# Kernel tuning notes

Hardware: AMD Instinct MI355X
Metric: run time of the kernel (lower is better)

## Reference

```python
import jax, jax.numpy as jnp
import numpy as np

ROI_SIZE = 7
MAX_BIN_H = 8   # max adaptive-maxpool bin height for crop H <= 37
MAX_BIN_W = 9   # max adaptive-maxpool bin width  for crop W <= 50
SCALE = 0.0625  # 1/16 feature stride


def setup_inputs() -> dict:
    key = jax.random.key(0)
    ks = jax.random.split(key, 12)
    B, C, h, w = 1, 512, 37, 50          # conv5 feature map of a 600x800 image
    N = 512                               # number of ROIs (proposals)
    n_class = 21
    d_in, d_fc = C * ROI_SIZE * ROI_SIZE, 4096
    x = jax.random.normal(ks[0], (B, C, h, w), dtype=jnp.float32)
    # rois in image coordinates (x1, y1, x2, y2), image is 800x600
    x1 = jax.random.uniform(ks[1], (N,), minval=0.0, maxval=700.0)
    y1 = jax.random.uniform(ks[2], (N,), minval=0.0, maxval=500.0)
    bw = jax.random.uniform(ks[3], (N,), minval=16.0, maxval=400.0)
    bh = jax.random.uniform(ks[4], (N,), minval=16.0, maxval=300.0)
    rois = jnp.stack([x1, y1, jnp.minimum(x1 + bw, 799.0), jnp.minimum(y1 + bh, 599.0)], axis=1).astype(jnp.float32)
    roi_index = jnp.zeros((N,), dtype=jnp.int32)  # single image in batch
    W1 = jax.random.normal(ks[5], (d_in, d_fc), dtype=jnp.float32) * 0.01
    b1 = jnp.zeros((d_fc,), dtype=jnp.float32)
    W2 = jax.random.normal(ks[6], (d_fc, d_fc), dtype=jnp.float32) * 0.01
    b2 = jnp.zeros((d_fc,), dtype=jnp.float32)
    Wp = jax.random.normal(ks[7], (d_fc, n_class * 4), dtype=jnp.float32) * 0.001
    bp = jax.random.normal(ks[8], (n_class * 4,), dtype=jnp.float32) * 0.001
    Ws = jax.random.normal(ks[9], (d_fc, n_class), dtype=jnp.float32) * 0.01
    bs = jax.random.normal(ks[10], (n_class,), dtype=jnp.float32) * 0.01
    return dict(x=x, rois=rois, roi_index=roi_index, W1=W1, b1=b1, W2=W2, b2=b2, Wp=Wp, bp=bp, Ws=Ws, bs=bs)


def _roi_pool(x, rois, roi_index):
    """Faithful port of roi_pooling(): per-ROI crop + AdaptiveMaxPool2d(7)."""
    B, C, h, w = x.shape
    S = ROI_SIZE
    coords = jnp.round(rois * SCALE)  # round-half-even, like torch.round
    cx1 = jnp.clip(coords[:, 0], 0, w).astype(jnp.int32)
    cy1 = jnp.clip(coords[:, 1], 0, h).astype(jnp.int32)
    cx2 = jnp.clip(coords[:, 2], 0, w).astype(jnp.int32)
    cy2 = jnp.clip(coords[:, 3], 0, h).astype(jnp.int32)
    bidx = roi_index.astype(jnp.int32)
    roi_stack = jnp.stack([bidx, cx1, cy1, cx2, cy2], axis=1)  # [N,5]

    def pool_one(carry, roi):
        bi, x1i, y1i, x2i, y2i = roi[0], roi[1], roi[2], roi[3], roi[4]
        valid = (x1i < x2i) & (y1i < y2i)
        # torch slicing roi[2]:roi[4]+1 silently truncates at the tensor edge
        x2e = jnp.minimum(x2i, w - 1)
        y2e = jnp.minimum(y2i, h - 1)
        Hc = y2e - y1i + 1
        Wc = x2e - x1i + 1
        i = jnp.arange(S)
        # adaptive max pool bins: [floor(i*H/S), ceil((i+1)*H/S))
        rs = y1i + (i * Hc) // S
        re = y1i + ((i + 1) * Hc + S - 1) // S
        cs = x1i + (i * Wc) // S
        ce = x1i + ((i + 1) * Wc + S - 1) // S
        rows = rs[:, None] + jnp.arange(MAX_BIN_H)          # [S, MBH]
        rmask = rows < re[:, None]
        rows = jnp.clip(rows, 0, h - 1)
        cols = cs[:, None] + jnp.arange(MAX_BIN_W)          # [S, MBW]
        cmask = cols < ce[:, None]
        cols = jnp.clip(cols, 0, w - 1)
        feat = x[bi]                                         # [C, h, w]
        g = feat[:, rows[:, None, :, None], cols[None, :, None, :]]  # [C,S,S,MBH,MBW]
        mask = rmask[:, None, :, None] & cmask[None, :, None, :]     # [S,S,MBH,MBW]
        pooled = jnp.where(mask, g, -jnp.inf).max(axis=(-2, -1))    # [C,S,S]
        pooled = jnp.where(valid, pooled, jnp.zeros_like(pooled))
        return carry, pooled

    _, out = jax.lax.scan(pool_one, None, roi_stack)  # [N, C, S, S]
    return out


def reference(x, rois, roi_index, W1, b1, W2, b2, Wp, bp, Ws, bs):
    pooled = _roi_pool(x, rois, roi_index)            # [N, 512, 7, 7]
    flat = pooled.reshape(pooled.shape[0], -1)        # [N, 25088]
    fc6 = jax.nn.relu(flat @ W1 + b1)                 # [N, 4096]
    fc7 = jax.nn.relu(fc6 @ W2 + b2)                  # [N, 4096]
    roi_class_params = fc7 @ Wp + bp                  # [N, n_class*4]
    roi_scores = fc7 @ Ws + bs                        # [N, n_class]
    return (roi_class_params, roi_scores)
```

## Files before the change

kernel.cpp:

```cpp
#include <hip/hip_runtime.h>
#include <hip/hip_bf16.h>

using f32x4  = float          __attribute__((ext_vector_type(4)));
using bf16x8 = __bf16         __attribute__((ext_vector_type(8)));
using u16x8  = unsigned short __attribute__((ext_vector_type(8)));

#define C_CH 512
#define H_IN 37
#define W_IN 50
#define NPOS 1850
#define NROI 512
#define DIN  25088
#define DFC  4096
#define NPAR 84
#define NCLS 21
#define KS_FC 4
#define KS_HEAD 16

#define PB_X  232
#define PB_WH 2048
#define PB_TOT (PB_X + PB_WH)

__device__ __forceinline__ unsigned pack_bf16x2(float a, float b) {
    __hip_bfloat162 h;
    h.x = __float2bfloat16(a);
    h.y = __float2bfloat16(b);
    return *reinterpret_cast<unsigned*>(&h);
}

__device__ __forceinline__ void gload_lds16(const void* src, void* dst) {
    __builtin_amdgcn_global_load_lds(
        (const __attribute__((address_space(1))) void*)src,
        (__attribute__((address_space(3))) void*)dst, 16, 0, 0);
}

__global__ __launch_bounds__(256) void prep_kernel(
        const float* __restrict__ x, float* __restrict__ xt,
        const float* __restrict__ Wp, const float* __restrict__ Ws,
        float* __restrict__ Whp) {
    __shared__ float tile[64][65];
    int b = blockIdx.x;
    int t = threadIdx.x;
    if (b < PB_X) {
        int p0 = (b % 29) * 64;
        int c0 = (b / 29) * 64;
        int tc = t & 63, tr = t >> 6;
#pragma unroll
        for (int i = 0; i < 16; ++i) {
            int r = tr + i * 4;
            int p = p0 + tc;
            float v = 0.f;
            if (p < NPOS) v = x[(size_t)(c0 + r) * NPOS + p];
            tile[r][tc] = v;
        }
        __syncthreads();
#pragma unroll
        for (int i = 0; i < 16; ++i) {
            int rw = tr + i * 4;
            int p = p0 + rw;
            if (p < NPOS) xt[(size_t)p * C_CH + c0 + tc] = tile[tc][rw];
        }
    } else {
        int idx = (b - PB_X) * 256 + t;
        int k = idx >> 7, c = idx & 127;
        float v = 0.f;
        if (c < NPAR) v = Wp[(size_t)k * NPAR + c];
        else if (c < NPAR + NCLS) v = Ws[(size_t)k * NCLS + (c - NPAR)];
        Whp[idx] = v;
    }
}

__global__ __launch_bounds__(256) void roi_pool_kernel(
        const float* __restrict__ xt, const float* __restrict__ rois,
        __hip_bfloat16* __restrict__ pooled) {
    int n = blockIdx.x;
    int t = threadIdx.x;
    float4 rv = reinterpret_cast<const float4*>(rois)[n];
    int x1 = (int)fminf(fmaxf(rintf(rv.x * 0.0625f), 0.f), (float)W_IN);
    int y1 = (int)fminf(fmaxf(rintf(rv.y * 0.0625f), 0.f), (float)H_IN);
    int x2 = (int)fminf(fmaxf(rintf(rv.z * 0.0625f), 0.f), (float)W_IN);
    int y2 = (int)fminf(fmaxf(rintf(rv.w * 0.0625f), 0.f), (float)H_IN);
    bool valid = (x1 < x2) && (y1 < y2);
    unsigned* outp = reinterpret_cast<unsigned*>(pooled) + (size_t)n * (DIN / 2);
    if (!valid) {
        for (int b = 0; b < 49; ++b) outp[b * 256 + t] = 0u;
        return;
    }
    int x2e = min(x2, W_IN - 1), y2e = min(y2, H_IN - 1);
    int Hc = y2e - y1 + 1, Wc = x2e - x1 + 1;
    const float2* base = reinterpret_cast<const float2*>(xt);
    for (int i = 0; i < 7; ++i) {
        int rs = y1 + (i * Hc) / 7;
        int re = y1 + ((i + 1) * Hc + 6) / 7;
        for (int j = 0; j < 7; ++j) {
            int cs = x1 + (j * Wc) / 7;
            int ce = x1 + ((j + 1) * Wc + 6) / 7;
            float m0 = -__builtin_inff(), m1 = -__builtin_inff();
            for (int r = rs; r < re; ++r) {
                const float2* rowp = base + (size_t)r * (W_IN * C_CH / 2) + t;
                for (int c = cs; c < ce; ++c) {
                    float2 v = rowp[c * (C_CH / 2)];
                    m0 = fmaxf(m0, v.x);
                    m1 = fmaxf(m1, v.y);
                }
            }
            outp[(i * 7 + j) * 256 + t] = pack_bf16x2(m0, m1);
        }
    }
}

__global__ __launch_bounds__(512) void gemm_m256_kernel(
        const __hip_bfloat16* __restrict__ A,
        const float* __restrict__ Bf,
        float* __restrict__ Cp,
        int N, int lda, int ldbn, int kChunk, int nMT, int nNT, int Mtot,
        int perm) {
    __shared__ __align__(16) char lA[3 * 32768];
    __shared__ __align__(16) char lB[2 * 16384];
    int q = gridDim.x >> 3;
    int bid = (blockIdx.x & 7) * q + (blockIdx.x >> 3);
    int mt = bid % nMT;
    int nt = (bid / nMT) % nNT;
    int ks = bid / (nMT * nNT);
    int m0 = mt * 256, n0 = nt * 128;
    int k0 = ks * kChunk;
    int t = threadIdx.x;
    int lane = t & 63, wid = t >> 6;

    const char* srcA[4]; int offA[4];
#pragma unroll
    for (int i = 0; i < 4; ++i) {
        int p = t * 16 + i * 8192;
        int row = p >> 7;
        int swz = ((row ^ (row >> 3)) & 7) << 4;
        srcA[i] = (const char*)A + ((size_t)(m0 + row) * lda + k0) * 2
                  + ((p & 127) ^ swz);
        offA[i] = p;
    }
    auto stageA = [&](int buf) {
#pragma unroll
        for (int i = 0; i < 4; ++i) {
            gload_lds16(srcA[i], lA + buf * 32768 + offA[i]);
            srcA[i] += 128;
        }
    };

    int n4 = (t & 31) * 4;
    int kq = (t >> 5) * 4;
    int woff[4];
#pragma unroll
    for (int j = 0; j < 4; ++j) {
        int row = n4 + j;
        int swz = ((row ^ (row >> 3)) & 7) << 4;
        woff[j] = row * 128 + ((kq * 2) ^ swz);
    }
    const float* Bbase = Bf + n0 + n4;
    f32x4 v[4];
    auto loadB = [&](int kt) {
        int kb = k0 + kt * 64;
        int rbase = perm ? ((kb & 511) * 49 + (kb >> 9)) : kb;
        int rstr  = perm ? 49 : 1;
#pragma unroll
        for (int p = 0; p < 4; ++p)
            v[p] = *reinterpret_cast<const f32x4*>(
                Bbase + (size_t)(rbase + (kq + p) * rstr) * ldbn);
    };
    auto cvtB = [&](int buf) {
#pragma unroll
        for (int j = 0; j < 4; ++j) {
            uint2 w;
            w.x = pack_bf16x2(v[0][j], v[1][j]);
            w.y = pack_bf16x2(v[2][j], v[3][j]);
            *reinterpret_cast<uint2*>(lB + buf * 16384 + woff[j]) = w;
        }
    };

    int wm = wid >> 1, wn = wid & 1;
    int kb0 = (lane >> 4) << 4;
    int roA[4], roB[4], sA[4], sB[4];
#pragma unroll
    for (int f = 0; f < 4; ++f) {
        int ra = wm * 64 + f * 16 + (lane & 15);
        roA[f] = ra * 128; sA[f] = ((ra ^ (ra >> 3)) & 7) << 4;
        int rb = wn * 64 + f * 16 + (lane & 15);
        roB[f] = rb * 128; sB[f] = ((rb ^ (rb >> 3)) & 7) << 4;
    }

    f32x4 acc[4][4] = {};
    auto mfmaStep = [&](int aBuf, int bBuf) {
        const char* baseA = lA + aBuf * 32768;
        const char* baseB = lB + bBuf * 16384;
#pragma unroll
        for (int ksub = 0; ksub < 2; ++ksub) {
            int kk = kb0 | (ksub << 6);
            bf16x8 af[4], bfr[4];
#pragma unroll
            for (int f = 0; f < 4; ++f)
                af[f] = *reinterpret_cast<const bf16x8*>(baseA + roA[f] + (kk ^ sA[f]));
#pragma unroll
            for (int f = 0; f < 4; ++f)
                bfr[f] = *reinterpret_cast<const bf16x8*>(baseB + roB[f] + (kk ^ sB[f]));
#pragma unroll
            for (int mf = 0; mf < 4; ++mf)
#pragma unroll
                for (int nf = 0; nf < 4; ++nf)
                    acc[mf][nf] = __builtin_amdgcn_mfma_f32_16x16x32_bf16(
                        af[mf], bfr[nf], acc[mf][nf], 0, 0, 0);
        }
    };

    int nkt = kChunk >> 6;

    stageA(0);
    stageA(1);
    loadB(0);
    cvtB(0);
    loadB(1);
    asm volatile("s_waitcnt vmcnt(4) lgkmcnt(0)\ns_barrier" ::: "memory");

    int aCur = 0, aStage = 2, bCur = 0;
    for (int kt = 0; kt + 2 < nkt; ++kt) {
        stageA(aStage);
        mfmaStep(aCur, bCur);
        cvtB(bCur ^ 1);
        loadB(kt + 2);
        asm volatile("s_waitcnt vmcnt(8) lgkmcnt(0)\ns_barrier" ::: "memory");
        aCur = aCur == 2 ? 0 : aCur + 1;
        aStage = aStage == 2 ? 0 : aStage + 1;
        bCur ^= 1;
    }
    mfmaStep(aCur, bCur);
    cvtB(bCur ^ 1);
    asm volatile("s_waitcnt vmcnt(0) lgkmcnt(0)\ns_barrier" ::: "memory");
    aCur = aCur == 2 ? 0 : aCur + 1;
    bCur ^= 1;
    mfmaStep(aCur, bCur);

    float* outp = Cp + (size_t)ks * Mtot * N;
    int rbase = m0 + wm * 64;
    int cbase = n0 + wn * 64 + (lane & 15);
    int rl = (lane >> 4) * 4;
#pragma unroll
    for (int mf = 0; mf < 4; ++mf)
#pragma unroll
        for (int nf = 0; nf < 4; ++nf)
#pragma unroll
            for (int r = 0; r < 4; ++r)
                outp[(size_t)(rbase + mf * 16 + rl + r) * N + cbase + nf * 16] =
                    acc[mf][nf][r];
}

__global__ __launch_bounds__(512, 2) void gemm_f32b_kernel(
        const __hip_bfloat16* __restrict__ A,
        const float* __restrict__ Bf,
        float* __restrict__ Cp,
        int N, int lda, int ldbn, int kChunk, int nMT, int nNT, int Mtot,
        int perm) {
    __shared__ __align__(16) char lA[3 * 16384];
    __shared__ __align__(16) char lB[2 * 16384];
    int q = gridDim.x >> 3;
    int bid = (blockIdx.x & 7) * q + (blockIdx.x >> 3);
    int mt = bid % nMT;
    int nt = (bid / nMT) % nNT;
    int ks = bid / (nMT * nNT);
    int m0 = mt * 128, n0 = nt * 128;
    int k0 = ks * kChunk;
    int t = threadIdx.x;
    int lane = t & 63, wid = t >> 6;

    const char* srcA[2]; int offA[2];
#pragma unroll
    for (int i = 0; i < 2; ++i) {
        int p = t * 16 + i * 8192;
        int row = p >> 7;
        int swz = ((row ^ (row >> 3)) & 7) << 4;
        srcA[i] = (const char*)A + ((size_t)(m0 + row) * lda + k0) * 2
                  + ((p & 127) ^ swz);
        offA[i] = p;
    }
    auto stageA = [&](int buf) {
#pragma unroll
        for (int i = 0; i < 2; ++i) {
            gload_lds16(srcA[i], lA + buf * 16384 + offA[i]);
            srcA[i] += 128;
        }
    };

    int n4 = (t & 31) * 4;
    int kq = (t >> 5) * 4;
    int woff[4];
#pragma unroll
    for (int j = 0; j < 4; ++j) {
        int row = n4 + j;
        int swz = ((row ^ (row >> 3)) & 7) << 4;
        woff[j] = row * 128 + ((kq * 2) ^ swz);
    }
    const float* Bbase = Bf + n0 + n4;
    f32x4 v[4];
    auto loadB = [&](int kt) {
        int kb = k0 + kt * 64;
        int rbase = perm ? ((kb & 511) * 49 + (kb >> 9)) : kb;
        int rstr  = perm ? 49 : 1;
#pragma unroll
        for (int p = 0; p < 4; ++p)
            v[p] = *reinterpret_cast<const f32x4*>(
                Bbase + (size_t)(rbase + (kq + p) * rstr) * ldbn);
    };
    auto cvtB = [&](int buf) {
#pragma unroll
        for (int j = 0; j < 4; ++j) {
            uint2 w;
            w.x = pack_bf16x2(v[0][j], v[1][j]);
            w.y = pack_bf16x2(v[2][j], v[3][j]);
            *reinterpret_cast<uint2*>(lB + buf * 16384 + woff[j]) = w;
        }
    };

    int wm = wid >> 2, wn = wid & 3;
    int kb0 = (lane >> 4) << 4;
    int roA[4], roB[2], sA[4], sB[2];
#pragma unroll
    for (int f = 0; f < 4; ++f) {
        int ra = wm * 64 + f * 16 + (lane & 15);
        roA[f] = ra * 128; sA[f] = ((ra ^ (ra >> 3)) & 7) << 4;
    }
#pragma unroll
    for (int f = 0; f < 2; ++f) {
        int rb = wn * 32 + f * 16 + (lane & 15);
        roB[f] = rb * 128; sB[f] = ((rb ^ (rb >> 3)) & 7) << 4;
    }

    f32x4 acc[4][2] = {};
    auto mfmaStep = [&](int aBuf, int bBuf) {
        const char* baseA = lA + aBuf * 16384;
        const char* baseB = lB + bBuf * 16384;
#pragma unroll
        for (int ksub = 0; ksub < 2; ++ksub) {
            int kk = kb0 | (ksub << 6);
            bf16x8 af[4], bfr[2];
#pragma unroll
            for (int f = 0; f < 4; ++f)
                af[f] = *reinterpret_cast<const bf16x8*>(baseA + roA[f] + (kk ^ sA[f]));
#pragma unroll
            for (int f = 0; f < 2; ++f)
                bfr[f] = *reinterpret_cast<const bf16x8*>(baseB + roB[f] + (kk ^ sB[f]));
#pragma unroll
            for (int mf = 0; mf < 4; ++mf)
#pragma unroll
                for (int nf = 0; nf < 2; ++nf)
                    acc[mf][nf] = __builtin_amdgcn_mfma_f32_16x16x32_bf16(
                        af[mf], bfr[nf], acc[mf][nf], 0, 0, 0);
        }
    };

    int nkt = kChunk >> 6;

    stageA(0);
    stageA(1);
    loadB(0);
    cvtB(0);
    loadB(1);
    asm volatile("s_waitcnt vmcnt(4) lgkmcnt(0)\ns_barrier" ::: "memory");

    int aCur = 0, aStage = 2, bCur = 0;
    for (int kt = 0; kt + 2 < nkt; ++kt) {
        stageA(aStage);
        mfmaStep(aCur, bCur);
        cvtB(bCur ^ 1);
        loadB(kt + 2);
        asm volatile("s_waitcnt vmcnt(6) lgkmcnt(0)\ns_barrier" ::: "memory");
        aCur = aCur == 2 ? 0 : aCur + 1;
        aStage = aStage == 2 ? 0 : aStage + 1;
        bCur ^= 1;
    }
    mfmaStep(aCur, bCur);
    cvtB(bCur ^ 1);
    asm volatile("s_waitcnt vmcnt(0) lgkmcnt(0)\ns_barrier" ::: "memory");
    aCur = aCur == 2 ? 0 : aCur + 1;
    bCur ^= 1;
    mfmaStep(aCur, bCur);

    float* outp = Cp + (size_t)ks * Mtot * N;
    int rbase = m0 + wm * 64;
    int cbase = n0 + wn * 32 + (lane & 15);
    int rl = (lane >> 4) * 4;
#pragma unroll
    for (int mf = 0; mf < 4; ++mf)
#pragma unroll
        for (int nf = 0; nf < 2; ++nf)
#pragma unroll
            for (int r = 0; r < 4; ++r)
                outp[(size_t)(rbase + mf * 16 + rl + r) * N + cbase + nf * 16] =
                    acc[mf][nf][r];
}

__global__ __launch_bounds__(256) void reduce_bias_relu_kernel(
        const float* __restrict__ P, const float* __restrict__ bias,
        __hip_bfloat16* __restrict__ out, int MN, int N, int KS) {
    int idx = blockIdx.x * blockDim.x + threadIdx.x;
    int e0 = idx * 4;
    if (e0 >= MN) return;
    f32x4 s = *reinterpret_cast<const f32x4*>(P + e0);
    for (int k = 1; k < KS; ++k)
        s += *reinterpret_cast<const f32x4*>(P + (size_t)k * MN + e0);
    f32x4 b = *reinterpret_cast<const f32x4*>(bias + (e0 & (N - 1)));
    s += b;
    uint2 pk;
    pk.x = pack_bf16x2(fmaxf(s[0], 0.f), fmaxf(s[1], 0.f));
    pk.y = pack_bf16x2(fmaxf(s[2], 0.f), fmaxf(s[3], 0.f));
    *reinterpret_cast<uint2*>(reinterpret_cast<char*>(out) + (size_t)e0 * 2) = pk;
}

__global__ __launch_bounds__(128) void head_reduce_kernel(
        const float* __restrict__ P, const float* __restrict__ bp,
        const float* __restrict__ bs, float* __restrict__ out) {
    int n = blockIdx.x, c = threadIdx.x;
    float s = 0.f;
#pragma unroll
    for (int ks = 0; ks < KS_HEAD; ++ks)
        s += P[(size_t)ks * NROI * 128 + (size_t)n * 128 + c];
    if (c < NPAR)
        out[(size_t)n * NPAR + c] = s + bp[c];
    else if (c < NPAR + NCLS)
        out[(size_t)NROI * NPAR + (size_t)n * NCLS + (c - NPAR)] = s + bs[c - NPAR];
}

extern "C" void kernel_launch(void* const* d_in, const int* in_sizes, int n_in,
                              void* d_out, int out_size, void* d_ws, size_t ws_size,
                              hipStream_t stream) {
    const float* x    = (const float*)d_in[0];
    const float* rois = (const float*)d_in[1];
    const float* W1 = (const float*)d_in[3];
    const float* b1 = (const float*)d_in[4];
    const float* W2 = (const float*)d_in[5];
    const float* b2 = (const float*)d_in[6];
    const float* Wp = (const float*)d_in[7];
    const float* bp = (const float*)d_in[8];
    const float* Ws = (const float*)d_in[9];
    const float* bs = (const float*)d_in[10];
    float* out = (float*)d_out;

    const size_t MB = 1ull << 20;
    char* ws = (char*)d_ws;
    float*          xt     = (float*)(ws + 0);
    __hip_bfloat16* pooled = (__hip_bfloat16*)(ws + 4   * MB);
    float*          Whp    = (float*)(ws + 30  * MB);
    float*          part   = (float*)(ws + 34  * MB);
    __hip_bfloat16* fc6    = (__hip_bfloat16*)(ws + 104 * MB);
    __hip_bfloat16* fc7    = (__hip_bfloat16*)(ws + 109 * MB);

    prep_kernel<<<PB_TOT, 256, 0, stream>>>(x, xt, Wp, Ws, Whp);
    roi_pool_kernel<<<NROI, 256, 0, stream>>>(xt, rois, pooled);

    gemm_m256_kernel<<<2 * 32 * KS_FC, 512, 0, stream>>>(
        pooled, W1, part, DFC, DIN, DFC, DIN / KS_FC, 2, 32, NROI, 1);
    reduce_bias_relu_kernel<<<2048, 256, 0, stream>>>(part, b1, fc6,
                                                      NROI * DFC, DFC, KS_FC);

    gemm_m256_kernel<<<2 * 32 * KS_FC, 512, 0, stream>>>(
        fc6, W2, part, DFC, DFC, DFC, DFC / KS_FC, 2, 32, NROI, 0);
    reduce_bias_relu_kernel<<<2048, 256, 0, stream>>>(part, b2, fc7,
                                                      NROI * DFC, DFC, KS_FC);

    gemm_f32b_kernel<<<4 * KS_HEAD, 512, 0, stream>>>(
        fc7, Whp, part, 128, DFC, 128, DFC / KS_HEAD, 4, 1, NROI, 0);
    head_reduce_kernel<<<NROI, 128, 0, stream>>>(part, bp, bs, out);
}
```

Baseline: 338.1 us.

## Use full-M 512x64 tiles in FC GEMMs so each weight tile is read once

The FC6/FC7 GEMM switches from 256x128 output tiles to tiles covering all 512 ROIs by 64 columns. Each fp32 weight element is now loaded and converted to bf16 by exactly one block, which halves weight traffic and conversion work. In exchange the activation tile is re-read by twice as many blocks. The A buffer drops from triple to double buffering at 128KB of LDS, which deepens per-block LDS use and lowers pipeline depth.

Result: slower. 395.8 us (+17.1%).

```diff
diff --git a/kernel.cpp b/kernel.cpp
--- a/kernel.cpp
+++ b/kernel.cpp
@@ -109,44 +109,42 @@
     }
 }
 
-__global__ __launch_bounds__(512) void gemm_m256_kernel(
+__global__ __launch_bounds__(512) void gemm_bm512_kernel(
         const __hip_bfloat16* __restrict__ A,
         const float* __restrict__ Bf,
         float* __restrict__ Cp,
-        int N, int lda, int ldbn, int kChunk, int nMT, int nNT, int Mtot,
-        int perm) {
-    __shared__ __align__(16) char lA[3 * 32768];
-    __shared__ __align__(16) char lB[2 * 16384];
+        int N, int lda, int ldbn, int kChunk, int nNT, int perm) {
+    __shared__ __align__(16) char lA[2 * 65536];
+    __shared__ __align__(16) char lB[2 * 8192];
     int q = gridDim.x >> 3;
     int bid = (blockIdx.x & 7) * q + (blockIdx.x >> 3);
-    int mt = bid % nMT;
-    int nt = (bid / nMT) % nNT;
-    int ks = bid / (nMT * nNT);
-    int m0 = mt * 256, n0 = nt * 128;
+    int nt = bid % nNT;
+    int ks = bid / nNT;
+    int n0 = nt * 64;
     int k0 = ks * kChunk;
     int t = threadIdx.x;
     int lane = t & 63, wid = t >> 6;
 
-    const char* srcA[4]; int offA[4];
-#pragma unroll
-    for (int i = 0; i < 4; ++i) {
+    const char* srcA[8]; int offA[8];
+#pragma unroll
+    for (int i = 0; i < 8; ++i) {
         int p = t * 16 + i * 8192;
         int row = p >> 7;
         int swz = ((row ^ (row >> 3)) & 7) << 4;
-        srcA[i] = (const char*)A + ((size_t)(m0 + row) * lda + k0) * 2
+        srcA[i] = (const char*)A + ((size_t)row * lda + k0) * 2
                   + ((p & 127) ^ swz);
         offA[i] = p;
     }
     auto stageA = [&](int buf) {
 #pragma unroll
-        for (int i = 0; i < 4; ++i) {
-            gload_lds16(srcA[i], lA + buf * 32768 + offA[i]);
+        for (int i = 0; i < 8; ++i) {
+            gload_lds16(srcA[i], lA + buf * 65536 + offA[i]);
             srcA[i] += 128;
         }
     };
 
-    int n4 = (t & 31) * 4;
-    int kq = (t >> 5) * 4;
+    int n4 = (t & 15) * 4;
+    int kq = (t >> 4) * 2;
     int woff[4];
 #pragma unroll
     for (int j = 0; j < 4; ++j) {
@@ -155,41 +153,37 @@
         woff[j] = row * 128 + ((kq * 2) ^ swz);
     }
     const float* Bbase = Bf + n0 + n4;
-    f32x4 v[4];
+    f32x4 v[2];
     auto loadB = [&](int kt) {
         int kb = k0 + kt * 64;
         int rbase = perm ? ((kb & 511) * 49 + (kb >> 9)) : kb;
         int rstr  = perm ? 49 : 1;
 #pragma unroll
-        for (int p = 0; p < 4; ++p)
+        for (int p = 0; p < 2; ++p)
             v[p] = *reinterpret_cast<const f32x4*>(
                 Bbase + (size_t)(rbase + (kq + p) * rstr) * ldbn);
     };
     auto cvtB = [&](int buf) {
 #pragma unroll
-        for (int j = 0; j < 4; ++j) {
-            uint2 w;
-            w.x = pack_bf16x2(v[0][j], v[1][j]);
-            w.y = pack_bf16x2(v[2][j], v[3][j]);
-            *reinterpret_cast<uint2*>(lB + buf * 16384 + woff[j]) = w;
-        }
-    };
-
-    int wm = wid >> 1, wn = wid & 1;
+        for (int j = 0; j < 4; ++j)
+            *reinterpret_cast<unsigned*>(lB + buf * 8192 + woff[j]) =
+                pack_bf16x2(v[0][j], v[1][j]);
+    };
+
     int kb0 = (lane >> 4) << 4;
     int roA[4], roB[4], sA[4], sB[4];
 #pragma unroll
     for (int f = 0; f < 4; ++f) {
-        int ra = wm * 64 + f * 16 + (lane & 15);
+        int ra = wid * 64 + f * 16 + (lane & 15);
         roA[f] = ra * 128; sA[f] = ((ra ^ (ra >> 3)) & 7) << 4;
-        int rb = wn * 64 + f * 16 + (lane & 15);
+        int rb = f * 16 + (lane & 15);
         roB[f] = rb * 128; sB[f] = ((rb ^ (rb >> 3)) & 7) << 4;
     }
 
     f32x4 acc[4][4] = {};
     auto mfmaStep = [&](int aBuf, int bBuf) {
-        const char* baseA = lA + aBuf * 32768;
-        const char* baseB = lB + bBuf * 16384;
+        const char* baseA = lA + aBuf * 65536;
+        const char* baseB = lB + bBuf * 8192;
 #pragma unroll
         for (int ksub = 0; ksub < 2; ++ksub) {
             int kk = kb0 | (ksub << 6);
@@ -212,33 +206,29 @@
     int nkt = kChunk >> 6;
 
     stageA(0);
-    stageA(1);
     loadB(0);
     cvtB(0);
     loadB(1);
-    asm volatile("s_waitcnt vmcnt(4) lgkmcnt(0)\ns_barrier" ::: "memory");
-
-    int aCur = 0, aStage = 2, bCur = 0;
-    for (int kt = 0; kt + 2 < nkt; ++kt) {
-        stageA(aStage);
+    asm volatile("s_waitcnt vmcnt(2) lgkmcnt(0)\ns_barrier" ::: "memory");
+
+    int aCur = 0, bCur = 0;
+    for (int kt = 0; kt < nkt; ++kt) {
+        if (kt + 1 < nkt) stageA(aCur ^ 1);
         mfmaStep(aCur, bCur);
-        cvtB(bCur ^ 1);
-        loadB(kt + 2);
-        asm volatile("s_waitcnt vmcnt(8) lgkmcnt(0)\ns_barrier" ::: "memory");
-        aCur = aCur == 2 ? 0 : aCur + 1;
-        aStage = aStage == 2 ? 0 : aStage + 1;
+        if (kt + 1 < nkt) cvtB(bCur ^ 1);
+        if (kt + 2 < nkt) {
+            loadB(kt + 2);
+            asm volatile("s_waitcnt vmcnt(2) lgkmcnt(0)\ns_barrier" ::: "memory");
+        } else {
+            asm volatile("s_waitcnt vmcnt(0) lgkmcnt(0)\ns_barrier" ::: "memory");
+        }
+        aCur ^= 1;
         bCur ^= 1;
     }
-    mfmaStep(aCur, bCur);
-    cvtB(bCur ^ 1);
-    asm volatile("s_waitcnt vmcnt(0) lgkmcnt(0)\ns_barrier" ::: "memory");
-    aCur = aCur == 2 ? 0 : aCur + 1;
-    bCur ^= 1;
-    mfmaStep(aCur, bCur);
-
-    float* outp = Cp + (size_t)ks * Mtot * N;
-    int rbase = m0 + wm * 64;
-    int cbase = n0 + wn * 64 + (lane & 15);
+
+    float* outp = Cp + (size_t)ks * NROI * N;
+    int rbase = wid * 64;
+    int cbase = n0 + (lane & 15);
     int rl = (lane >> 4) * 4;
 #pragma unroll
     for (int mf = 0; mf < 4; ++mf)
@@ -452,13 +442,13 @@
     prep_kernel<<<PB_TOT, 256, 0, stream>>>(x, xt, Wp, Ws, Whp);
     roi_pool_kernel<<<NROI, 256, 0, stream>>>(xt, rois, pooled);
 
-    gemm_m256_kernel<<<2 * 32 * KS_FC, 512, 0, stream>>>(
-        pooled, W1, part, DFC, DIN, DFC, DIN / KS_FC, 2, 32, NROI, 1);
+    gemm_bm512_kernel<<<64 * KS_FC, 512, 0, stream>>>(
+        pooled, W1, part, DFC, DIN, DFC, DIN / KS_FC, 64, 1);
     reduce_bias_relu_kernel<<<2048, 256, 0, stream>>>(part, b1, fc6,
                                                       NROI * DFC, DFC, KS_FC);
 
-    gemm_m256_kernel<<<2 * 32 * KS_FC, 512, 0, stream>>>(
-        fc6, W2, part, DFC, DFC, DFC, DFC / KS_FC, 2, 32, NROI, 0);
+    gemm_bm512_kernel<<<64 * KS_FC, 512, 0, stream>>>(
+        fc6, W2, part, DFC, DFC, DFC, DFC / KS_FC, 64, 0);
     reduce_bias_relu_kernel<<<2048, 256, 0, stream>>>(part, b2, fc7,
                                                       NROI * DFC, DFC, KS_FC);
 
```
